# Performance work log

Hardware: AMD Instinct MI355X
Metric: run time of the kernel (lower is better)

Reference implementation:

```python
import jax, jax.numpy as jnp
import numpy as np

EXP_EMBD = 1024
EXP_Q_H = 8
EXP_HEAD_DIM = 256
EXP_KV_H = 1
EXP_KV_DIM = EXP_KV_H * EXP_HEAD_DIM  # 256
EXP_FFN = 4096
B, L, LC = 8, 512, 2048


def setup_inputs() -> dict:
    key = jax.random.key(0)
    ks = jax.random.split(key, 12)
    def w(k, shape):
        fan_in = shape[-1]
        return jax.random.normal(k, shape, jnp.float32) * (fan_in ** -0.5)
    return {
        "x": jax.random.normal(ks[0], (B, L, EXP_EMBD), jnp.float32),
        "text_k": jax.random.normal(ks[1], (B, LC, EXP_KV_DIM), jnp.float32),
        "text_v": jax.random.normal(ks[2], (B, LC, EXP_KV_DIM), jnp.float32),
        "ln1_w": jnp.ones((EXP_EMBD,), jnp.float32),
        "ln2_w": jnp.ones((EXP_EMBD,), jnp.float32),
        "Wq": w(ks[3], (EXP_Q_H * EXP_HEAD_DIM, EXP_EMBD)),
        "Wk": w(ks[4], (EXP_KV_DIM, EXP_KV_DIM)),
        "Wv": w(ks[5], (EXP_KV_DIM, EXP_KV_DIM)),
        "Wo": w(ks[6], (EXP_EMBD, EXP_Q_H * EXP_HEAD_DIM)),
        "Wg": w(ks[7], (EXP_FFN, EXP_EMBD)),
        "Wu": w(ks[8], (EXP_FFN, EXP_EMBD)),
        "Wd": w(ks[9], (EXP_EMBD, EXP_FFN)),
    }


def _rmsnorm(x, w):
    # torch.nn.RMSNorm with eps=None -> eps = finfo(dtype).eps
    eps = jnp.asarray(jnp.finfo(jnp.float32).eps, x.dtype)
    return x * jax.lax.rsqrt(jnp.mean(x * x, axis=-1, keepdims=True) + eps) * w


def _rope(x):
    # x: [B, L, H, D]
    b, l, h, d = x.shape
    d2 = d // 2
    ts = 10000.0 ** (2.0 / d * jnp.arange(d2, dtype=jnp.float32))  # [d2]
    rad = jnp.arange(l, dtype=jnp.float32)[:, None] / ts[None, :]  # [L, d2]
    s = jnp.sin(rad)[None, :, None, :]
    c = jnp.cos(rad)[None, :, None, :]
    x1, x2 = x[..., :d2], x[..., d2:]
    return jnp.concatenate([x1 * c - x2 * s, x2 * c + x1 * s], axis=-1)


def reference(x, text_k, text_v, ln1_w, ln2_w, Wq, Wk, Wv, Wo, Wg, Wu, Wd):
    b, l, _ = x.shape
    lc = text_k.shape[1]
    residual = x
    h = _rmsnorm(x, ln1_w)
    q = _rope((h @ Wq.T).reshape(b, l, EXP_Q_H, EXP_HEAD_DIM))          # [B,L,QH,D]
    k = (text_k @ Wk.T).reshape(b, lc, EXP_KV_H, EXP_HEAD_DIM)          # [B,Lc,KVH,D]
    v = (text_v @ Wv.T).reshape(b, lc, EXP_KV_H, EXP_HEAD_DIM)
    kv_map = (jnp.arange(EXP_Q_H) * EXP_KV_H) // EXP_Q_H                # GQA head map
    kh = jnp.take(k, kv_map, axis=2)                                    # [B,Lc,QH,D]
    vh = jnp.take(v, kv_map, axis=2)
    scale = 1.0 / np.sqrt(EXP_HEAD_DIM).astype(np.float32)
    scores = jnp.einsum('blhd,bchd->bhlc', q, kh) * scale               # [B,QH,L,Lc]
    attn = jax.nn.softmax(scores, axis=-1)
    ctx = jnp.einsum('bhlc,bchd->blhd', attn, vh).reshape(b, l, -1)
    x = ctx @ Wo.T + residual
    residual = x
    h = _rmsnorm(x, ln2_w)
    return (jax.nn.silu(h @ Wg.T) * (h @ Wu.T)) @ Wd.T + residual
```

## Files before the change

### kernel.cpp

```cpp
#include <hip/hip_runtime.h>

typedef __attribute__((ext_vector_type(4))) float f32x4;
typedef __attribute__((ext_vector_type(8))) short s16x8;
typedef __attribute__((ext_vector_type(4))) unsigned short u16x4;

#define B_    8
#define L_    512
#define LC_   2048
#define EMBD  1024

__device__ __forceinline__ float b2f(unsigned short u) {
  unsigned int i = ((unsigned int)u) << 16;
  float f; __builtin_memcpy(&f, &i, 4); return f;
}
__device__ __forceinline__ unsigned short f2b(float f) {
  unsigned int i; __builtin_memcpy(&i, &f, 4);
  unsigned int r = i + 0x7FFFu + ((i >> 16) & 1u);
  return (unsigned short)(r >> 16);
}

#define GLL16(g, l)                                                         \
  __builtin_amdgcn_global_load_lds(                                         \
      (__attribute__((address_space(1))) void*)(g),                         \
      (__attribute__((address_space(3))) void*)(l), 16, 0, 0)

#define VMCNT6() asm volatile("s_waitcnt vmcnt(6)" ::: "memory")
#define VMCNT0() asm volatile("s_waitcnt vmcnt(0)" ::: "memory")
#define LGKM0()  asm volatile("s_waitcnt lgkmcnt(0)" ::: "memory")

__global__ __launch_bounds__(256) void convert9(
    const float* s0, const float* s1, const float* s2, const float* s3,
    const float* s4, const float* s5, const float* s6, const float* s7,
    const float* s8,
    unsigned short* d0, unsigned short* d1, unsigned short* d2,
    unsigned short* d3, unsigned short* d4, unsigned short* d5,
    unsigned short* d6, unsigned short* d7, unsigned short* d8) {
  int bk = blockIdx.x;
  const float* s; unsigned short* d; int base;
  if      (bk <  2048) { s = s0; d = d0; base = 0; }
  else if (bk <  2112) { s = s1; d = d1; base = 2048; }
  else if (bk <  2176) { s = s2; d = d2; base = 2112; }
  else if (bk <  4224) { s = s3; d = d3; base = 2176; }
  else if (bk <  8320) { s = s4; d = d4; base = 4224; }
  else if (bk < 12416) { s = s5; d = d5; base = 8320; }
  else if (bk < 16512) { s = s6; d = d6; base = 12416; }
  else if (bk < 20608) { s = s7; d = d7; base = 16512; }
  else                 { s = s8; d = d8; base = 20608; }
  int i = (bk - base) * 256 + threadIdx.x;
  float4 v = ((const float4*)s)[i];
  u16x4 o = { f2b(v.x), f2b(v.y), f2b(v.z), f2b(v.w) };
  ((u16x4*)d)[i] = o;
}

__global__ __launch_bounds__(256) void rmsnorm_kernel(
    const float* __restrict__ x, const float* __restrict__ w,
    unsigned short* __restrict__ out) {
  int row = blockIdx.x;
  int tid = threadIdx.x;
  float4 v = ((const float4*)(x + (size_t)row * EMBD))[tid];
  float ss = v.x*v.x + v.y*v.y + v.z*v.z + v.w*v.w;
#pragma unroll
  for (int o = 1; o < 64; o <<= 1) ss += __shfl_xor(ss, o);
  __shared__ float red[4];
  if ((tid & 63) == 0) red[tid >> 6] = ss;
  __syncthreads();
  float tot = red[0] + red[1] + red[2] + red[3];
  float rs = rsqrtf(tot * (1.0f / EMBD) + 1.1920928955078125e-07f);
  float4 wv = ((const float4*)w)[tid];
  u16x4 o = { f2b(v.x*rs*wv.x), f2b(v.y*rs*wv.y), f2b(v.z*rs*wv.z), f2b(v.w*rs*wv.w) };
  ((u16x4*)(out + (size_t)row * EMBD))[tid] = o;
}

__global__ __launch_bounds__(256) void rope_kernel(unsigned short* __restrict__ q) {
  int idx = blockIdx.x * 256 + threadIdx.x;
  int i   = idx & 127;
  int h   = (idx >> 7) & 7;
  int row = idx >> 10;
  int l   = row & (L_ - 1);
  size_t base = (size_t)row * 2048 + h * 256 + i;
  float x1 = b2f(q[base]);
  float x2 = b2f(q[base + 128]);
  float ts  = powf(10000.0f, (float)i * (2.0f / 256.0f));
  float rad = (float)l / ts;
  float s, c;
  sincosf(rad, &s, &c);
  q[base]       = f2b(x1 * c - x2 * s);
  q[base + 128] = f2b(x2 * c + x1 * s);
}

__global__ __launch_bounds__(256) void act_kernel(
    const unsigned short* __restrict__ g, const unsigned short* __restrict__ u,
    unsigned short* __restrict__ out, int n8) {
  int i = blockIdx.x * 256 + threadIdx.x;
  if (i >= n8) return;
  s16x8 gv = ((const s16x8*)g)[i];
  s16x8 uv = ((const s16x8*)u)[i];
  s16x8 ov;
#pragma unroll
  for (int j = 0; j < 8; ++j) {
    float gf = b2f((unsigned short)gv[j]);
    float uf = b2f((unsigned short)uv[j]);
    float s  = gf / (1.0f + __expf(-gf));
    ov[j] = (short)f2b(s * uf);
  }
  ((s16x8*)out)[i] = ov;
}

template <int ADD_RES, int OUT_BF16>
__global__ __launch_bounds__(256, 2) void gemm_nt(
    const unsigned short* __restrict__ A, const unsigned short* __restrict__ Bw,
    const float* __restrict__ Res, void* __restrict__ C, int M, int N, int K) {
  __shared__ unsigned short As[128 * 64];
  __shared__ unsigned short Bs[128 * 64];
  const int tid = threadIdx.x;
  const int lane = tid & 63, wid = tid >> 6;
  const int l15 = lane & 15, l4 = lane >> 4;
  const int wr = wid >> 1, wc = wid & 1;
  const int m0 = blockIdx.y * 128, n0 = blockIdx.x * 128;

  const f32x4 fz = {0.f, 0.f, 0.f, 0.f};
  f32x4 acc[4][4];
#pragma unroll
  for (int i = 0; i < 4; ++i)
#pragma unroll
    for (int j = 0; j < 4; ++j) acc[i][j] = fz;

  for (int k0 = 0; k0 < K; k0 += 64) {
    __syncthreads();
#pragma unroll
    for (int i = 0; i < 4; ++i) {
      int Li = i * 4096 + tid * 16;
      int row = Li >> 7;
      int kb = (Li & 127) ^ ((row & 7) << 4);
      GLL16((const char*)(A + (size_t)(m0 + row) * K + k0) + kb, (char*)As + Li);
      GLL16((const char*)(Bw + (size_t)(n0 + row) * K + k0) + kb, (char*)Bs + Li);
    }
    __syncthreads();
#pragma unroll
    for (int kk = 0; kk < 2; ++kk) {
      s16x8 af[4], bfr[4];
#pragma unroll
      for (int mi = 0; mi < 4; ++mi) {
        int row = wr * 64 + mi * 16 + l15;
        int kb = (kk * 64 + l4 * 16) ^ ((row & 7) << 4);
        af[mi] = *(const s16x8*)((const char*)As + row * 128 + kb);
      }
#pragma unroll
      for (int ni = 0; ni < 4; ++ni) {
        int row = wc * 64 + ni * 16 + l15;
        int kb = (kk * 64 + l4 * 16) ^ ((row & 7) << 4);
        bfr[ni] = *(const s16x8*)((const char*)Bs + row * 128 + kb);
      }
#pragma unroll
      for (int mi = 0; mi < 4; ++mi)
#pragma unroll
        for (int ni = 0; ni < 4; ++ni)
          acc[mi][ni] = __builtin_amdgcn_mfma_f32_16x16x32_bf16(
              af[mi], bfr[ni], acc[mi][ni], 0, 0, 0);
    }
  }
#pragma unroll
  for (int mi = 0; mi < 4; ++mi) {
#pragma unroll
    for (int r = 0; r < 4; ++r) {
      int grow = m0 + wr * 64 + mi * 16 + l4 * 4 + r;
      size_t base = (size_t)grow * N + n0 + wc * 64 + l15;
#pragma unroll
      for (int ni = 0; ni < 4; ++ni) {
        float v = acc[mi][ni][r];
        size_t idx = base + ni * 16;
        if (ADD_RES) v += Res[idx];
        if (OUT_BF16) ((unsigned short*)C)[idx] = f2b(v);
        else          ((float*)C)[idx] = v;
      }
    }
  }
}

template <int ADD_RES, int OUT_BF16>
__global__ __launch_bounds__(256, 2) void gemm_nt64(
    const unsigned short* __restrict__ A, const unsigned short* __restrict__ Bw,
    const float* __restrict__ Res, void* __restrict__ C, int M, int N, int K) {
  __shared__ unsigned short As[64 * 64];
  __shared__ unsigned short Bs[128 * 64];
  const int tid = threadIdx.x;
  const int lane = tid & 63, wid = tid >> 6;
  const int l15 = lane & 15, l4 = lane >> 4;
  const int wr = wid >> 1, wc = wid & 1;
  const int m0 = blockIdx.y * 64, n0 = blockIdx.x * 128;

  const f32x4 fz = {0.f, 0.f, 0.f, 0.f};
  f32x4 acc[2][4];
#pragma unroll
  for (int i = 0; i < 2; ++i)
#pragma unroll
    for (int j = 0; j < 4; ++j) acc[i][j] = fz;

  for (int k0 = 0; k0 < K; k0 += 64) {
    __syncthreads();
#pragma unroll
    for (int i = 0; i < 2; ++i) {
      int Li = i * 4096 + tid * 16;
      int row = Li >> 7;
      int kb = (Li & 127) ^ ((row & 7) << 4);
      GLL16((const char*)(A + (size_t)(m0 + row) * K + k0) + kb, (char*)As + Li);
    }
#pragma unroll
    for (int i = 0; i < 4; ++i) {
      int Li = i * 4096 + tid * 16;
      int row = Li >> 7;
      int kb = (Li & 127) ^ ((row & 7) << 4);
      GLL16((const char*)(Bw + (size_t)(n0 + row) * K + k0) + kb, (char*)Bs + Li);
    }
    __syncthreads();
#pragma unroll
    for (int kk = 0; kk < 2; ++kk) {
      s16x8 af[2], bfr[4];
#pragma unroll
      for (int mi = 0; mi < 2; ++mi) {
        int row = wr * 32 + mi * 16 + l15;
        int kb = (kk * 64 + l4 * 16) ^ ((row & 7) << 4);
        af[mi] = *(const s16x8*)((const char*)As + row * 128 + kb);
      }
#pragma unroll
      for (int ni = 0; ni < 4; ++ni) {
        int row = wc * 64 + ni * 16 + l15;
        int kb = (kk * 64 + l4 * 16) ^ ((row & 7) << 4);
        bfr[ni] = *(const s16x8*)((const char*)Bs + row * 128 + kb);
      }
#pragma unroll
      for (int mi = 0; mi < 2; ++mi)
#pragma unroll
        for (int ni = 0; ni < 4; ++ni)
          acc[mi][ni] = __builtin_amdgcn_mfma_f32_16x16x32_bf16(
              af[mi], bfr[ni], acc[mi][ni], 0, 0, 0);
    }
  }
#pragma unroll
  for (int mi = 0; mi < 2; ++mi) {
#pragma unroll
    for (int r = 0; r < 4; ++r) {
      int grow = m0 + wr * 32 + mi * 16 + l4 * 4 + r;
      size_t base = (size_t)grow * N + n0 + wc * 64 + l15;
#pragma unroll
      for (int ni = 0; ni < 4; ++ni) {
        float v = acc[mi][ni][r];
        size_t idx = base + ni * 16;
        if (ADD_RES) v += Res[idx];
        if (OUT_BF16) ((unsigned short*)C)[idx] = f2b(v);
        else          ((float*)C)[idx] = v;
      }
    }
  }
}

__global__ __launch_bounds__(512, 2) void gemm256(
    const unsigned short* __restrict__ A, const unsigned short* __restrict__ Bw,
    unsigned short* __restrict__ C, int M, int N, int K) {
  extern __shared__ char smem[];
  const int tid = threadIdx.x;
  const int lane = tid & 63;
  const int wid = tid >> 6;
  const int wr = wid >> 2, wc = wid & 3;
  const int l15 = lane & 15, g = lane >> 4;
  int flat = blockIdx.y * 16 + blockIdx.x;
  flat = (flat & 7) * 32 + (flat >> 3);
  const int m0 = (flat >> 4) * 256, n0 = (flat & 15) * 256;
  const int T = K >> 6;
  const int swz = (l15 & 7) << 4;

  auto stage = [&](int t, int mat, int half) {
    char* dst = smem + mat * 65536 + (t & 1) * 32768 + half * 16384;
    const unsigned short* src = (mat ? Bw + (size_t)(n0 + half * 128) * K
                                     : A + (size_t)(m0 + half * 128) * K) + t * 64;
#pragma unroll
    for (int i = 0; i < 2; ++i) {
      int Li = i * 8192 + tid * 16;
      int row = Li >> 7;
      int kb = (Li & 127) ^ ((row & 7) << 4);
      GLL16((const char*)(src + (size_t)row * K) + kb, dst + Li);
    }
  };

  const f32x4 fz = {0.f, 0.f, 0.f, 0.f};
  f32x4 acc[2][2][4][2];
#pragma unroll
  for (int ms = 0; ms < 2; ++ms)
#pragma unroll
    for (int ns = 0; ns < 2; ++ns)
#pragma unroll
      for (int mi = 0; mi < 4; ++mi)
#pragma unroll
        for (int ni = 0; ni < 2; ++ni) acc[ms][ns][mi][ni] = fz;

  stage(0, 1, 0); stage(0, 1, 1); stage(0, 0, 0); stage(0, 0, 1);
  stage(1, 1, 0); stage(1, 1, 1); stage(1, 0, 0);
  VMCNT6();
  __builtin_amdgcn_s_barrier();

  for (int t = 0; t < T; ++t) {
    char* Ab = smem + (t & 1) * 32768 + wr * 16384;
    char* Bb = smem + 65536 + (t & 1) * 32768 + (wc >> 1) * 16384;
    const int bn = (wc & 1) * 64;
    s16x8 a[4][2], b0[2][2], b1[2][2];

#pragma unroll
    for (int mi = 0; mi < 4; ++mi) {
      int row = mi * 16 + l15;
#pragma unroll
      for (int kk = 0; kk < 2; ++kk)
        a[mi][kk] = *(const s16x8*)(Ab + row * 128 + ((kk * 64 + g * 16) ^ swz));
    }
#pragma unroll
    for (int ni = 0; ni < 2; ++ni) {
      int r0 = (bn + ni * 16 + l15) * 128;
      int r1 = (bn + 32 + ni * 16 + l15) * 128;
#pragma unroll
      for (int kk = 0; kk < 2; ++kk) {
        int ko = (kk * 64 + g * 16) ^ swz;
        b0[ni][kk] = *(const s16x8*)(Bb + r0 + ko);
        b1[ni][kk] = *(const s16x8*)(Bb + r1 + ko);
      }
    }
    if (t + 1 < T) stage(t + 1, 0, 1);
    __builtin_amdgcn_s_barrier();
    LGKM0();
    __builtin_amdgcn_sched_barrier(0);
    __builtin_amdgcn_s_setprio(1);
#pragma unroll
    for (int mi = 0; mi < 4; ++mi)
#pragma unroll
      for (int ni = 0; ni < 2; ++ni)
#pragma unroll
        for (int kk = 0; kk < 2; ++kk)
          acc[0][0][mi][ni] = __builtin_amdgcn_mfma_f32_16x16x32_bf16(
              a[mi][kk], b0[ni][kk], acc[0][0][mi][ni], 0, 0, 0);
    __builtin_amdgcn_s_setprio(0);
    __builtin_amdgcn_s_barrier();

    if (t + 2 < T) stage(t + 2, 1, 0);
    __builtin_amdgcn_s_barrier();
    __builtin_amdgcn_s_setprio(1);
#pragma unroll
    for (int mi = 0; mi < 4; ++mi)
#pragma unroll
      for (int ni = 0; ni < 2; ++ni)
#pragma unroll
        for (int kk = 0; kk < 2; ++kk)
          acc[0][1][mi][ni] = __builtin_amdgcn_mfma_f32_16x16x32_bf16(
              a[mi][kk], b1[ni][kk], acc[0][1][mi][ni], 0, 0, 0);
    __builtin_amdgcn_s_setprio(0);
    __builtin_amdgcn_s_barrier();

#pragma unroll
    for (int mi = 0; mi < 4; ++mi) {
      int row = 64 + mi * 16 + l15;
#pragma unroll
      for (int kk = 0; kk < 2; ++kk)
        a[mi][kk] = *(const s16x8*)(Ab + row * 128 + ((kk * 64 + g * 16) ^ swz));
    }
    if (t + 2 < T) stage(t + 2, 1, 1);
    __builtin_amdgcn_s_barrier();
    LGKM0();
    __builtin_amdgcn_sched_barrier(0);
    __builtin_amdgcn_s_setprio(1);
#pragma unroll
    for (int mi = 0; mi < 4; ++mi)
#pragma unroll
      for (int ni = 0; ni < 2; ++ni)
#pragma unroll
        for (int kk = 0; kk < 2; ++kk)
          acc[1][0][mi][ni] = __builtin_amdgcn_mfma_f32_16x16x32_bf16(
              a[mi][kk], b0[ni][kk], acc[1][0][mi][ni], 0, 0, 0);
    __builtin_amdgcn_s_setprio(0);
    __builtin_amdgcn_s_barrier();

    if (t + 2 < T) { stage(t + 2, 0, 0); VMCNT6(); }
    else           { VMCNT0(); }
    __builtin_amdgcn_s_barrier();
    __builtin_amdgcn_s_setprio(1);
#pragma unroll
    for (int mi = 0; mi < 4; ++mi)
#pragma unroll
      for (int ni = 0; ni < 2; ++ni)
#pragma unroll
        for (int kk = 0; kk < 2; ++kk)
          acc[1][1][mi][ni] = __builtin_amdgcn_mfma_f32_16x16x32_bf16(
              a[mi][kk], b1[ni][kk], acc[1][1][mi][ni], 0, 0, 0);
    __builtin_amdgcn_s_setprio(0);
    __builtin_amdgcn_s_barrier();
  }

#pragma unroll
  for (int ms = 0; ms < 2; ++ms)
#pragma unroll
    for (int mi = 0; mi < 4; ++mi)
#pragma unroll
      for (int r = 0; r < 4; ++r) {
        int grow = m0 + wr * 128 + ms * 64 + mi * 16 + g * 4 + r;
        size_t base = (size_t)grow * N + n0 + wc * 64;
#pragma unroll
        for (int ns = 0; ns < 2; ++ns)
#pragma unroll
          for (int ni = 0; ni < 2; ++ni)
            C[base + ns * 32 + ni * 16 + l15] = f2b(acc[ms][ns][mi][ni][r]);
      }
}

#define SWZV(d) (((((d) & 7) ^ (((d) >> 3) & 7))) << 4)

__global__ __launch_bounds__(512, 2) void attn_kernel(
    const unsigned short* __restrict__ Q,
    const unsigned short* __restrict__ Kc,
    const unsigned short* __restrict__ Vc,
    unsigned short* __restrict__ Op0, unsigned short* __restrict__ Op1,
    float2* __restrict__ Ml0, float2* __restrict__ Ml1) {
  __shared__ unsigned short Ks[64 * 256];
  __shared__ unsigned short Vt[256 * 64];
  const int tid = threadIdx.x;
  const int lane = tid & 63, wid = tid >> 6;
  const int l15 = lane & 15, g = lane >> 4;
  const int qt = blockIdx.x, h = blockIdx.y;
  const int b = blockIdx.z >> 1, half = blockIdx.z & 1;

  const size_t qrow = (size_t)(b * L_ + qt * 128 + wid * 16 + l15);
  const unsigned short* qp = Q + qrow * 2048 + h * 256;
  s16x8 qf[8];
#pragma unroll
  for (int kc = 0; kc < 8; ++kc) qf[kc] = *(const s16x8*)(qp + kc * 32 + g * 8);

  const f32x4 fz = {0.f, 0.f, 0.f, 0.f};
  f32x4 oacc[16];
#pragma unroll
  for (int i = 0; i < 16; ++i) oacc[i] = fz;
  float m_run = -__builtin_inff(), l_run = 0.f;

  const unsigned short* Kb = Kc + (size_t)b * LC_ * 256;
  const unsigned short* Vb = Vc + (size_t)b * LC_ * 256;

  const int kt0 = half * 16;
  for (int kt = kt0; kt < kt0 + 16; ++kt) {
    __syncthreads();
#pragma unroll
    for (int i = 0; i < 4; ++i) {
      int Li = i * 8192 + tid * 16;
      int row = Li >> 9;
      int kb = (Li & 511) ^ ((row & 7) << 4);
      GLL16((const char*)(Kb + (size_t)(kt * 64 + row) * 256) + kb, (char*)Ks + Li);
    }
#pragma unroll
    for (int p = 0; p < 2; ++p) {
      int id = p * 512 + tid;
      int dgrp = id & 31;
      int kvp = id >> 5;
      int d0 = dgrp * 8, kv0 = kvp * 2;
      const unsigned short* v0p = Vb + (size_t)(kt * 64 + kv0) * 256 + d0;
      s16x8 r0 = *(const s16x8*)v0p;
      s16x8 r1 = *(const s16x8*)(v0p + 256);
#pragma unroll
      for (int j = 0; j < 8; ++j) {
        int d = d0 + j;
        unsigned int val = (unsigned int)(unsigned short)r0[j] |
                           ((unsigned int)(unsigned short)r1[j] << 16);
        *(unsigned int*)((char*)Vt + d * 128 + ((kv0 * 2) ^ SWZV(d))) = val;
      }
    }
    __syncthreads();

    f32x4 sacc[4];
#pragma unroll
    for (int mi = 0; mi < 4; ++mi) sacc[mi] = fz;
#pragma unroll
    for (int mi = 0; mi < 4; ++mi) {
      int row = mi * 16 + l15;
      int swz = (row & 7) << 4;
#pragma unroll
      for (int kc = 0; kc < 8; ++kc) {
        s16x8 kf = *(const s16x8*)((const char*)Ks + row * 512 + ((kc * 64 + g * 16) ^ swz));
        sacc[mi] = __builtin_amdgcn_mfma_f32_16x16x32_bf16(kf, qf[kc], sacc[mi], 0, 0, 0);
      }
    }
    float sv[4][4];
    float mt = -__builtin_inff();
#pragma unroll
    for (int mi = 0; mi < 4; ++mi)
#pragma unroll
      for (int r = 0; r < 4; ++r) {
        float t = sacc[mi][r] * 0.0625f;
        sv[mi][r] = t;
        mt = fmaxf(mt, t);
      }
    mt = fmaxf(mt, __shfl_xor(mt, 16));
    mt = fmaxf(mt, __shfl_xor(mt, 32));
    if (!__all(mt <= m_run + 8.0f)) {
      float mnew = fmaxf(m_run, mt);
      float alpha = __expf(m_run - mnew);
      float af4[4];
#pragma unroll
      for (int r = 0; r < 4; ++r) af4[r] = __shfl(alpha, g * 4 + r);
#pragma unroll
      for (int nd = 0; nd < 16; ++nd)
#pragma unroll
        for (int r = 0; r < 4; ++r) oacc[nd][r] *= af4[r];
      l_run *= alpha;
      m_run = mnew;
    }
    float rs = 0.f;
#pragma unroll
    for (int mi = 0; mi < 4; ++mi)
#pragma unroll
      for (int r = 0; r < 4; ++r) {
        float p = __expf(sv[mi][r] - m_run);
        sv[mi][r] = p;
        rs += p;
      }
    rs += __shfl_xor(rs, 16);
    rs += __shfl_xor(rs, 32);
    l_run += rs;
    unsigned int pk[4][2];
#pragma unroll
    for (int ni = 0; ni < 4; ++ni) {
      pk[ni][0] = (unsigned int)f2b(sv[ni][0]) | ((unsigned int)f2b(sv[ni][1]) << 16);
      pk[ni][1] = (unsigned int)f2b(sv[ni][2]) | ((unsigned int)f2b(sv[ni][3]) << 16);
    }
    int cbase = (g & 1) << 3;
#pragma unroll
    for (int tt = 0; tt < 2; ++tt) {
      unsigned int w[4];
#pragma unroll
      for (int jj = 0; jj < 4; ++jj) {
        int c = cbase + (jj << 1);
        int src = ((c >> 2) << 4) + l15;
        unsigned int ra = __shfl(pk[2 * tt][jj & 1], src);
        unsigned int rb = __shfl(pk[2 * tt + 1][jj & 1], src);
        w[jj] = (g < 2) ? ra : rb;
      }
      union { unsigned int u[4]; s16x8 v; } cvt;
      cvt.u[0] = w[0]; cvt.u[1] = w[1]; cvt.u[2] = w[2]; cvt.u[3] = w[3];
      s16x8 ap = cvt.v;
#pragma unroll
      for (int nd = 0; nd < 16; ++nd) {
        int d = nd * 16 + l15;
        s16x8 vf = *(const s16x8*)((const char*)Vt + d * 128 + ((tt * 64 + g * 16) ^ SWZV(d)));
        oacc[nd] = __builtin_amdgcn_mfma_f32_16x16x32_bf16(ap, vf, oacc[nd], 0, 0, 0);
      }
    }
  }
  unsigned short* Op = half ? Op1 : Op0;
  float2* Ml = half ? Ml1 : Ml0;
  float lf[4];
#pragma unroll
  for (int r = 0; r < 4; ++r) lf[r] = 1.0f / __shfl(l_run, g * 4 + r);
  const size_t orow0 = (size_t)(b * L_ + qt * 128 + wid * 16);
#pragma unroll
  for (int r = 0; r < 4; ++r) {
    size_t base = (orow0 + g * 4 + r) * 2048 + h * 256 + l15;
#pragma unroll
    for (int nd = 0; nd < 16; ++nd)
      Op[base + nd * 16] = f2b(oacc[nd][r] * lf[r]);
  }
  if (g == 0) Ml[(orow0 + l15) * 8 + h] = make_float2(m_run, l_run);
}

__global__ __launch_bounds__(256) void attn_merge(
    const unsigned short* __restrict__ p0, const unsigned short* __restrict__ p1,
    const float2* __restrict__ ml0, const float2* __restrict__ ml1,
    unsigned short* __restrict__ ctx) {
  int i = blockIdx.x * 256 + threadIdx.x;
  int rowh = i >> 5;
  int dch = i & 31;
  float2 a = ml0[rowh], c = ml1[rowh];
  float M = fmaxf(a.x, c.x);
  float w0 = a.y * __expf(a.x - M), w1 = c.y * __expf(c.x - M);
  float inv = 1.0f / (w0 + w1);
  w0 *= inv; w1 *= inv;
  int row = rowh >> 3, h = rowh & 7;
  size_t off = (size_t)row * 2048 + h * 256 + dch * 8;
  s16x8 v0 = *(const s16x8*)(p0 + off);
  s16x8 v1 = *(const s16x8*)(p1 + off);
  s16x8 o;
#pragma unroll
  for (int j = 0; j < 8; ++j)
    o[j] = (short)f2b(w0 * b2f((unsigned short)v0[j]) + w1 * b2f((unsigned short)v1[j]));
  *(s16x8*)(ctx + off) = o;
}

extern "C" void kernel_launch(void* const* d_in, const int* in_sizes, int n_in,
                              void* d_out, int out_size, void* d_ws, size_t ws_size,
                              hipStream_t stream) {
  const float* x   = (const float*)d_in[0];
  const float* tk  = (const float*)d_in[1];
  const float* tv  = (const float*)d_in[2];
  const float* ln1 = (const float*)d_in[3];
  const float* ln2 = (const float*)d_in[4];
  const float* Wq  = (const float*)d_in[5];
  const float* Wk  = (const float*)d_in[6];
  const float* Wv  = (const float*)d_in[7];
  const float* Wo  = (const float*)d_in[8];
  const float* Wg  = (const float*)d_in[9];
  const float* Wu  = (const float*)d_in[10];
  const float* Wd  = (const float*)d_in[11];
  float* out = (float*)d_out;
  char* ws = (char*)d_ws;

  (void)hipFuncSetAttribute((const void*)gemm256,
                            hipFuncAttributeMaxDynamicSharedMemorySize, 131072);

  unsigned short* tk_bf  = (unsigned short*)(ws + 0);
  unsigned short* tv_bf  = (unsigned short*)(ws + 8388608);
  unsigned short* k_bf   = (unsigned short*)(ws + 16777216);
  unsigned short* v_bf   = (unsigned short*)(ws + 25165824);
  unsigned short* g_bf   = (unsigned short*)(ws + 0);
  unsigned short* op0    = (unsigned short*)(ws + 0);
  unsigned short* q_bf   = (unsigned short*)(ws + 33554432);
  unsigned short* ctx_bf = (unsigned short*)(ws + 50331648);
  unsigned short* u_bf   = (unsigned short*)(ws + 33554432);
  unsigned short* wq_bf  = (unsigned short*)(ws + 67108864);
  unsigned short* wk_bf  = (unsigned short*)(ws + 71303168);
  unsigned short* wv_bf  = (unsigned short*)(ws + 71434240);
  unsigned short* wo_bf  = (unsigned short*)(ws + 71565312);
  unsigned short* wg_bf  = (unsigned short*)(ws + 75759616);
  unsigned short* wu_bf  = (unsigned short*)(ws + 84148224);
  unsigned short* wd_bf  = (unsigned short*)(ws + 92536832);
  unsigned short* h_bf   = (unsigned short*)(ws + 100925440);
  float2*         ml0    = (float2*)(ws + 100925440);
  float2*         ml1    = (float2*)(ws + 100925440 + 262144);
  float*          x2     = (float*)(ws + 109314048);
  unsigned short* op1    = (unsigned short*)(ws + 109314048);

  dim3 blk(256);
  convert9<<<dim3(24704), blk, 0, stream>>>(
      Wq, Wk, Wv, Wo, Wg, Wu, Wd, tk, tv,
      wq_bf, wk_bf, wv_bf, wo_bf, wg_bf, wu_bf, wd_bf, tk_bf, tv_bf);

  rmsnorm_kernel<<<dim3(4096), blk, 0, stream>>>(x, ln1, h_bf);
  gemm_nt<0, 1><<<dim3(16, 32), blk, 0, stream>>>(h_bf, wq_bf, nullptr, q_bf, 4096, 2048, 1024);
  rope_kernel<<<dim3(16384), blk, 0, stream>>>(q_bf);
  gemm_nt64<0, 1><<<dim3(2, 256), blk, 0, stream>>>(tk_bf, wk_bf, nullptr, k_bf, 16384, 256, 256);
  gemm_nt64<0, 1><<<dim3(2, 256), blk, 0, stream>>>(tv_bf, wv_bf, nullptr, v_bf, 16384, 256, 256);
  attn_kernel<<<dim3(4, 8, 16), dim3(512), 0, stream>>>(q_bf, k_bf, v_bf, op0, op1, ml0, ml1);
  attn_merge<<<dim3(4096), blk, 0, stream>>>(op0, op1, ml0, ml1, ctx_bf);
  gemm_nt64<1, 0><<<dim3(8, 64), blk, 0, stream>>>(ctx_bf, wo_bf, x, x2, 4096, 1024, 2048);
  rmsnorm_kernel<<<dim3(4096), blk, 0, stream>>>(x2, ln2, h_bf);
  gemm256<<<dim3(16, 16), dim3(512), 131072, stream>>>(h_bf, wg_bf, g_bf, 4096, 4096, 1024);
  gemm256<<<dim3(16, 16), dim3(512), 131072, stream>>>(h_bf, wu_bf, u_bf, 4096, 4096, 1024);
  act_kernel<<<dim3(8192), blk, 0, stream>>>(g_bf, u_bf, g_bf, 2097152);
  gemm_nt64<1, 0><<<dim3(8, 64), blk, 0, stream>>>(g_bf, wd_bf, x2, out, 4096, 1024, 4096);
}
```

Before: 411.6 us.

## Process two 16-row query tiles per wave in attention kernel with 256 threads

Each attention wave now handles 32 query rows, two independent 16-row tiles, instead of 16. The workgroup shrinks from 512 to 256 threads, so the same 128-row block is covered by half as many waves. Each K and V fragment read from LDS now feeds two MFMAs, halving LDS read traffic per unit of compute and giving independent MFMA chains to interleave. The cost is roughly double the accumulator registers per wave (two 16x256 output tiles), which may hurt occupancy or cause spills, and each thread now does twice as many global loads for K and V per tile.

```diff
diff --git a/kernel.cpp b/kernel.cpp
--- a/kernel.cpp
+++ b/kernel.cpp
@@ -409,7 +409,7 @@
 
 #define SWZV(d) (((((d) & 7) ^ (((d) >> 3) & 7))) << 4)
 
-__global__ __launch_bounds__(512, 2) void attn_kernel(
+__global__ __launch_bounds__(256, 2) void attn_kernel(
     const unsigned short* __restrict__ Q,
     const unsigned short* __restrict__ Kc,
     const unsigned short* __restrict__ Vc,
@@ -423,17 +423,22 @@
   const int qt = blockIdx.x, h = blockIdx.y;
   const int b = blockIdx.z >> 1, half = blockIdx.z & 1;
 
-  const size_t qrow = (size_t)(b * L_ + qt * 128 + wid * 16 + l15);
-  const unsigned short* qp = Q + qrow * 2048 + h * 256;
-  s16x8 qf[8];
-#pragma unroll
-  for (int kc = 0; kc < 8; ++kc) qf[kc] = *(const s16x8*)(qp + kc * 32 + g * 8);
+  const size_t qrowA = (size_t)(b * L_ + qt * 128 + wid * 32 + l15);
+  const unsigned short* qpA = Q + qrowA * 2048 + h * 256;
+  const unsigned short* qpB = qpA + 16 * 2048;
+  s16x8 qfA[8], qfB[8];
+#pragma unroll
+  for (int kc = 0; kc < 8; ++kc) {
+    qfA[kc] = *(const s16x8*)(qpA + kc * 32 + g * 8);
+    qfB[kc] = *(const s16x8*)(qpB + kc * 32 + g * 8);
+  }
 
   const f32x4 fz = {0.f, 0.f, 0.f, 0.f};
-  f32x4 oacc[16];
-#pragma unroll
-  for (int i = 0; i < 16; ++i) oacc[i] = fz;
-  float m_run = -__builtin_inff(), l_run = 0.f;
+  f32x4 oaccA[16], oaccB[16];
+#pragma unroll
+  for (int i = 0; i < 16; ++i) { oaccA[i] = fz; oaccB[i] = fz; }
+  float m_runA = -__builtin_inff(), l_runA = 0.f;
+  float m_runB = -__builtin_inff(), l_runB = 0.f;
 
   const unsigned short* Kb = Kc + (size_t)b * LC_ * 256;
   const unsigned short* Vb = Vc + (size_t)b * LC_ * 256;
@@ -442,15 +447,15 @@
   for (int kt = kt0; kt < kt0 + 16; ++kt) {
     __syncthreads();
 #pragma unroll
-    for (int i = 0; i < 4; ++i) {
-      int Li = i * 8192 + tid * 16;
+    for (int i = 0; i < 8; ++i) {
+      int Li = i * 4096 + tid * 16;
       int row = Li >> 9;
       int kb = (Li & 511) ^ ((row & 7) << 4);
       GLL16((const char*)(Kb + (size_t)(kt * 64 + row) * 256) + kb, (char*)Ks + Li);
     }
 #pragma unroll
-    for (int p = 0; p < 2; ++p) {
-      int id = p * 512 + tid;
+    for (int p = 0; p < 4; ++p) {
+      int id = p * 256 + tid;
       int dgrp = id & 31;
       int kvp = id >> 5;
       int d0 = dgrp * 8, kv0 = kvp * 2;
@@ -467,9 +472,9 @@
     }
     __syncthreads();
 
-    f32x4 sacc[4];
-#pragma unroll
-    for (int mi = 0; mi < 4; ++mi) sacc[mi] = fz;
+    f32x4 sA[4], sB[4];
+#pragma unroll
+    for (int mi = 0; mi < 4; ++mi) { sA[mi] = fz; sB[mi] = fz; }
 #pragma unroll
     for (int mi = 0; mi < 4; ++mi) {
       int row = mi * 16 + l15;
@@ -477,89 +482,152 @@
 #pragma unroll
       for (int kc = 0; kc < 8; ++kc) {
         s16x8 kf = *(const s16x8*)((const char*)Ks + row * 512 + ((kc * 64 + g * 16) ^ swz));
-        sacc[mi] = __builtin_amdgcn_mfma_f32_16x16x32_bf16(kf, qf[kc], sacc[mi], 0, 0, 0);
-      }
-    }
-    float sv[4][4];
-    float mt = -__builtin_inff();
-#pragma unroll
-    for (int mi = 0; mi < 4; ++mi)
-#pragma unroll
-      for (int r = 0; r < 4; ++r) {
-        float t = sacc[mi][r] * 0.0625f;
-        sv[mi][r] = t;
-        mt = fmaxf(mt, t);
-      }
-    mt = fmaxf(mt, __shfl_xor(mt, 16));
-    mt = fmaxf(mt, __shfl_xor(mt, 32));
-    if (!__all(mt <= m_run + 8.0f)) {
-      float mnew = fmaxf(m_run, mt);
-      float alpha = __expf(m_run - mnew);
-      float af4[4];
-#pragma unroll
-      for (int r = 0; r < 4; ++r) af4[r] = __shfl(alpha, g * 4 + r);
-#pragma unroll
-      for (int nd = 0; nd < 16; ++nd)
-#pragma unroll
-        for (int r = 0; r < 4; ++r) oacc[nd][r] *= af4[r];
-      l_run *= alpha;
-      m_run = mnew;
-    }
-    float rs = 0.f;
-#pragma unroll
-    for (int mi = 0; mi < 4; ++mi)
-#pragma unroll
-      for (int r = 0; r < 4; ++r) {
-        float p = __expf(sv[mi][r] - m_run);
-        sv[mi][r] = p;
-        rs += p;
-      }
-    rs += __shfl_xor(rs, 16);
-    rs += __shfl_xor(rs, 32);
-    l_run += rs;
-    unsigned int pk[4][2];
-#pragma unroll
-    for (int ni = 0; ni < 4; ++ni) {
-      pk[ni][0] = (unsigned int)f2b(sv[ni][0]) | ((unsigned int)f2b(sv[ni][1]) << 16);
-      pk[ni][1] = (unsigned int)f2b(sv[ni][2]) | ((unsigned int)f2b(sv[ni][3]) << 16);
-    }
+        sA[mi] = __builtin_amdgcn_mfma_f32_16x16x32_bf16(kf, qfA[kc], sA[mi], 0, 0, 0);
+        sB[mi] = __builtin_amdgcn_mfma_f32_16x16x32_bf16(kf, qfB[kc], sB[mi], 0, 0, 0);
+      }
+    }
+
+    float svA[4][4], svB[4][4];
+    unsigned int pkA[4][2], pkB[4][2];
+    {
+      float mt = -__builtin_inff();
+#pragma unroll
+      for (int mi = 0; mi < 4; ++mi)
+#pragma unroll
+        for (int r = 0; r < 4; ++r) {
+          float t = sA[mi][r] * 0.0625f;
+          svA[mi][r] = t;
+          mt = fmaxf(mt, t);
+        }
+      mt = fmaxf(mt, __shfl_xor(mt, 16));
+      mt = fmaxf(mt, __shfl_xor(mt, 32));
+      if (!__all(mt <= m_runA + 8.0f)) {
+        float mnew = fmaxf(m_runA, mt);
+        float alpha = __expf(m_runA - mnew);
+        float af4[4];
+#pragma unroll
+        for (int r = 0; r < 4; ++r) af4[r] = __shfl(alpha, g * 4 + r);
+#pragma unroll
+        for (int nd = 0; nd < 16; ++nd)
+#pragma unroll
+          for (int r = 0; r < 4; ++r) oaccA[nd][r] *= af4[r];
+        l_runA *= alpha;
+        m_runA = mnew;
+      }
+      float rs = 0.f;
+#pragma unroll
+      for (int mi = 0; mi < 4; ++mi)
+#pragma unroll
+        for (int r = 0; r < 4; ++r) {
+          float p = __expf(svA[mi][r] - m_runA);
+          svA[mi][r] = p;
+          rs += p;
+        }
+      rs += __shfl_xor(rs, 16);
+      rs += __shfl_xor(rs, 32);
+      l_runA += rs;
+#pragma unroll
+      for (int ni = 0; ni < 4; ++ni) {
+        pkA[ni][0] = (unsigned int)f2b(svA[ni][0]) | ((unsigned int)f2b(svA[ni][1]) << 16);
+        pkA[ni][1] = (unsigned int)f2b(svA[ni][2]) | ((unsigned int)f2b(svA[ni][3]) << 16);
+      }
+    }
+    {
+      float mt = -__builtin_inff();
+#pragma unroll
+      for (int mi = 0; mi < 4; ++mi)
+#pragma unroll
+        for (int r = 0; r < 4; ++r) {
+          float t = sB[mi][r] * 0.0625f;
+          svB[mi][r] = t;
+          mt = fmaxf(mt, t);
+        }
+      mt = fmaxf(mt, __shfl_xor(mt, 16));
+      mt = fmaxf(mt, __shfl_xor(mt, 32));
+      if (!__all(mt <= m_runB + 8.0f)) {
+        float mnew = fmaxf(m_runB, mt);
+        float alpha = __expf(m_runB - mnew);
+        float af4[4];
+#pragma unroll
+        for (int r = 0; r < 4; ++r) af4[r] = __shfl(alpha, g * 4 + r);
+#pragma unroll
+        for (int nd = 0; nd < 16; ++nd)
+#pragma unroll
+          for (int r = 0; r < 4; ++r) oaccB[nd][r] *= af4[r];
+        l_runB *= alpha;
+        m_runB = mnew;
+      }
+      float rs = 0.f;
+#pragma unroll
+      for (int mi = 0; mi < 4; ++mi)
+#pragma unroll
+        for (int r = 0; r < 4; ++r) {
+          float p = __expf(svB[mi][r] - m_runB);
+          svB[mi][r] = p;
+          rs += p;
+        }
+      rs += __shfl_xor(rs, 16);
+      rs += __shfl_xor(rs, 32);
+      l_runB += rs;
+#pragma unroll
+      for (int ni = 0; ni < 4; ++ni) {
+        pkB[ni][0] = (unsigned int)f2b(svB[ni][0]) | ((unsigned int)f2b(svB[ni][1]) << 16);
+        pkB[ni][1] = (unsigned int)f2b(svB[ni][2]) | ((unsigned int)f2b(svB[ni][3]) << 16);
+      }
+    }
+
     int cbase = (g & 1) << 3;
 #pragma unroll
     for (int tt = 0; tt < 2; ++tt) {
-      unsigned int w[4];
+      unsigned int wA[4], wB[4];
 #pragma unroll
       for (int jj = 0; jj < 4; ++jj) {
         int c = cbase + (jj << 1);
         int src = ((c >> 2) << 4) + l15;
-        unsigned int ra = __shfl(pk[2 * tt][jj & 1], src);
-        unsigned int rb = __shfl(pk[2 * tt + 1][jj & 1], src);
-        w[jj] = (g < 2) ? ra : rb;
-      }
-      union { unsigned int u[4]; s16x8 v; } cvt;
-      cvt.u[0] = w[0]; cvt.u[1] = w[1]; cvt.u[2] = w[2]; cvt.u[3] = w[3];
-      s16x8 ap = cvt.v;
+        unsigned int raA = __shfl(pkA[2 * tt][jj & 1], src);
+        unsigned int rbA = __shfl(pkA[2 * tt + 1][jj & 1], src);
+        wA[jj] = (g < 2) ? raA : rbA;
+        unsigned int raB = __shfl(pkB[2 * tt][jj & 1], src);
+        unsigned int rbB = __shfl(pkB[2 * tt + 1][jj & 1], src);
+        wB[jj] = (g < 2) ? raB : rbB;
+      }
+      union { unsigned int u[4]; s16x8 v; } cvA, cvB;
+      cvA.u[0] = wA[0]; cvA.u[1] = wA[1]; cvA.u[2] = wA[2]; cvA.u[3] = wA[3];
+      cvB.u[0] = wB[0]; cvB.u[1] = wB[1]; cvB.u[2] = wB[2]; cvB.u[3] = wB[3];
+      s16x8 apA = cvA.v, apB = cvB.v;
 #pragma unroll
       for (int nd = 0; nd < 16; ++nd) {
         int d = nd * 16 + l15;
         s16x8 vf = *(const s16x8*)((const char*)Vt + d * 128 + ((tt * 64 + g * 16) ^ SWZV(d)));
-        oacc[nd] = __builtin_amdgcn_mfma_f32_16x16x32_bf16(ap, vf, oacc[nd], 0, 0, 0);
+        oaccA[nd] = __builtin_amdgcn_mfma_f32_16x16x32_bf16(apA, vf, oaccA[nd], 0, 0, 0);
+        oaccB[nd] = __builtin_amdgcn_mfma_f32_16x16x32_bf16(apB, vf, oaccB[nd], 0, 0, 0);
       }
     }
   }
   unsigned short* Op = half ? Op1 : Op0;
   float2* Ml = half ? Ml1 : Ml0;
-  float lf[4];
-#pragma unroll
-  for (int r = 0; r < 4; ++r) lf[r] = 1.0f / __shfl(l_run, g * 4 + r);
-  const size_t orow0 = (size_t)(b * L_ + qt * 128 + wid * 16);
+  const size_t orow0A = (size_t)(b * L_ + qt * 128 + wid * 32);
+  const size_t orow0B = orow0A + 16;
+  float lfA[4], lfB[4];
 #pragma unroll
   for (int r = 0; r < 4; ++r) {
-    size_t base = (orow0 + g * 4 + r) * 2048 + h * 256 + l15;
-#pragma unroll
-    for (int nd = 0; nd < 16; ++nd)
-      Op[base + nd * 16] = f2b(oacc[nd][r] * lf[r]);
-  }
-  if (g == 0) Ml[(orow0 + l15) * 8 + h] = make_float2(m_run, l_run);
+    lfA[r] = 1.0f / __shfl(l_runA, g * 4 + r);
+    lfB[r] = 1.0f / __shfl(l_runB, g * 4 + r);
+  }
+#pragma unroll
+  for (int r = 0; r < 4; ++r) {
+    size_t baseA = (orow0A + g * 4 + r) * 2048 + h * 256 + l15;
+    size_t baseB = (orow0B + g * 4 + r) * 2048 + h * 256 + l15;
+#pragma unroll
+    for (int nd = 0; nd < 16; ++nd) {
+      Op[baseA + nd * 16] = f2b(oaccA[nd][r] * lfA[r]);
+      Op[baseB + nd * 16] = f2b(oaccB[nd][r] * lfB[r]);
+    }
+  }
+  if (g == 0) {
+    Ml[(orow0A + l15) * 8 + h] = make_float2(m_runA, l_runA);
+    Ml[(orow0B + l15) * 8 + h] = make_float2(m_runB, l_runB);
+  }
 }
 
 __global__ __launch_bounds__(256) void attn_merge(
@@ -638,7 +706,7 @@
   rope_kernel<<<dim3(16384), blk, 0, stream>>>(q_bf);
   gemm_nt64<0, 1><<<dim3(2, 256), blk, 0, stream>>>(tk_bf, wk_bf, nullptr, k_bf, 16384, 256, 256);
   gemm_nt64<0, 1><<<dim3(2, 256), blk, 0, stream>>>(tv_bf, wv_bf, nullptr, v_bf, 16384, 256, 256);
-  attn_kernel<<<dim3(4, 8, 16), dim3(512), 0, stream>>>(q_bf, k_bf, v_bf, op0, op1, ml0, ml1);
+  attn_kernel<<<dim3(4, 8, 16), dim3(256), 0, stream>>>(q_bf, k_bf, v_bf, op0, op1, ml0, ml1);
   attn_merge<<<dim3(4096), blk, 0, stream>>>(op0, op1, ml0, ml1, ctx_bf);
   gemm_nt64<1, 0><<<dim3(8, 64), blk, 0, stream>>>(ctx_bf, wo_bf, x, x2, 4096, 1024, 2048);
   rmsnorm_kernel<<<dim3(4096), blk, 0, stream>>>(x2, ln2, h_bf);
```

Measured after the change: 688.1 us. +67.2%, slower.

## Double-buffer K/V tiles in attention and fuse SwiGLU into up-projection GEMM epilogue

Applied to the files above, without the earlier changes.

The attention kernel now uses 128KB of dynamic shared memory with two K and two V tile buffers. The next tile's K is fetched asynchronously and its V is loaded into registers while the current tile's MFMAs run, leaving one barrier per iteration. Separately, the SiLU-gate multiply moves into the epilogue of the up-projection GEMM, which reads the gate output and overwrites it in place. This drops the standalone activation kernel and one bf16 intermediate round trip. The larger shared memory footprint may cut attention occupancy from two blocks per CU to one.

```diff
diff --git a/kernel.cpp b/kernel.cpp
--- a/kernel.cpp
+++ b/kernel.cpp
@@ -88,24 +88,6 @@
   q[base + 128] = f2b(x2 * c + x1 * s);
 }
 
-__global__ __launch_bounds__(256) void act_kernel(
-    const unsigned short* __restrict__ g, const unsigned short* __restrict__ u,
-    unsigned short* __restrict__ out, int n8) {
-  int i = blockIdx.x * 256 + threadIdx.x;
-  if (i >= n8) return;
-  s16x8 gv = ((const s16x8*)g)[i];
-  s16x8 uv = ((const s16x8*)u)[i];
-  s16x8 ov;
-#pragma unroll
-  for (int j = 0; j < 8; ++j) {
-    float gf = b2f((unsigned short)gv[j]);
-    float uf = b2f((unsigned short)uv[j]);
-    float s  = gf / (1.0f + __expf(-gf));
-    ov[j] = (short)f2b(s * uf);
-  }
-  ((s16x8*)out)[i] = ov;
-}
-
 template <int ADD_RES, int OUT_BF16>
 __global__ __launch_bounds__(256, 2) void gemm_nt(
     const unsigned short* __restrict__ A, const unsigned short* __restrict__ Bw,
@@ -254,9 +236,11 @@
   }
 }
 
+template <int SWIGLU>
 __global__ __launch_bounds__(512, 2) void gemm256(
     const unsigned short* __restrict__ A, const unsigned short* __restrict__ Bw,
-    unsigned short* __restrict__ C, int M, int N, int K) {
+    const unsigned short* __restrict__ G, unsigned short* __restrict__ C,
+    int M, int N, int K) {
   extern __shared__ char smem[];
   const int tid = threadIdx.x;
   const int lane = tid & 63;
@@ -402,8 +386,15 @@
 #pragma unroll
         for (int ns = 0; ns < 2; ++ns)
 #pragma unroll
-          for (int ni = 0; ni < 2; ++ni)
-            C[base + ns * 32 + ni * 16 + l15] = f2b(acc[ms][ns][mi][ni][r]);
+          for (int ni = 0; ni < 2; ++ni) {
+            size_t idx = base + ns * 32 + ni * 16 + l15;
+            float v = acc[ms][ns][mi][ni][r];
+            if (SWIGLU) {
+              float gf = b2f(G[idx]);
+              v *= gf / (1.0f + __expf(-gf));
+            }
+            C[idx] = f2b(v);
+          }
       }
 }
 
@@ -415,8 +406,7 @@
     const unsigned short* __restrict__ Vc,
     unsigned short* __restrict__ Op0, unsigned short* __restrict__ Op1,
     float2* __restrict__ Ml0, float2* __restrict__ Ml1) {
-  __shared__ unsigned short Ks[64 * 256];
-  __shared__ unsigned short Vt[256 * 64];
+  extern __shared__ char ats[];
   const int tid = threadIdx.x;
   const int lane = tid & 63, wid = tid >> 6;
   const int l15 = lane & 15, g = lane >> 4;
@@ -438,34 +428,55 @@
   const unsigned short* Kb = Kc + (size_t)b * LC_ * 256;
   const unsigned short* Vb = Vc + (size_t)b * LC_ * 256;
 
-  const int kt0 = half * 16;
-  for (int kt = kt0; kt < kt0 + 16; ++kt) {
-    __syncthreads();
+  auto stageK = [&](int kt, char* dstK) {
 #pragma unroll
     for (int i = 0; i < 4; ++i) {
       int Li = i * 8192 + tid * 16;
       int row = Li >> 9;
       int kb = (Li & 511) ^ ((row & 7) << 4);
-      GLL16((const char*)(Kb + (size_t)(kt * 64 + row) * 256) + kb, (char*)Ks + Li);
-    }
+      GLL16((const char*)(Kb + (size_t)(kt * 64 + row) * 256) + kb, dstK + Li);
+    }
+  };
+  s16x8 vr[2][2];
+  auto loadV = [&](int kt) {
 #pragma unroll
     for (int p = 0; p < 2; ++p) {
       int id = p * 512 + tid;
-      int dgrp = id & 31;
-      int kvp = id >> 5;
+      int dgrp = id & 31, kvp = id >> 5;
+      const unsigned short* v0p = Vb + (size_t)(kt * 64 + kvp * 2) * 256 + dgrp * 8;
+      vr[p][0] = *(const s16x8*)v0p;
+      vr[p][1] = *(const s16x8*)(v0p + 256);
+    }
+  };
+  auto writeV = [&](char* dstV) {
+#pragma unroll
+    for (int p = 0; p < 2; ++p) {
+      int id = p * 512 + tid;
+      int dgrp = id & 31, kvp = id >> 5;
       int d0 = dgrp * 8, kv0 = kvp * 2;
-      const unsigned short* v0p = Vb + (size_t)(kt * 64 + kv0) * 256 + d0;
-      s16x8 r0 = *(const s16x8*)v0p;
-      s16x8 r1 = *(const s16x8*)(v0p + 256);
 #pragma unroll
       for (int j = 0; j < 8; ++j) {
         int d = d0 + j;
-        unsigned int val = (unsigned int)(unsigned short)r0[j] |
-                           ((unsigned int)(unsigned short)r1[j] << 16);
-        *(unsigned int*)((char*)Vt + d * 128 + ((kv0 * 2) ^ SWZV(d))) = val;
-      }
-    }
-    __syncthreads();
+        unsigned int val = (unsigned int)(unsigned short)vr[p][0][j] |
+                           ((unsigned int)(unsigned short)vr[p][1][j] << 16);
+        *(unsigned int*)(dstV + d * 128 + ((kv0 * 2) ^ SWZV(d))) = val;
+      }
+    }
+  };
+
+  const int kt0 = half * 16, ktE = kt0 + 16;
+  stageK(kt0, ats);
+  loadV(kt0);
+  VMCNT0();
+  writeV(ats + 65536);
+  __syncthreads();
+
+  for (int kt = kt0; kt < ktE; ++kt) {
+    const int cur = (kt - kt0) & 1, nxt = cur ^ 1;
+    char* KsB = ats + cur * 32768;
+    char* VtB = ats + 65536 + cur * 32768;
+    const bool more = (kt + 1 < ktE);
+    if (more) { stageK(kt + 1, ats + nxt * 32768); loadV(kt + 1); }
 
     f32x4 sacc[4];
 #pragma unroll
@@ -476,7 +487,7 @@
       int swz = (row & 7) << 4;
 #pragma unroll
       for (int kc = 0; kc < 8; ++kc) {
-        s16x8 kf = *(const s16x8*)((const char*)Ks + row * 512 + ((kc * 64 + g * 16) ^ swz));
+        s16x8 kf = *(const s16x8*)(KsB + row * 512 + ((kc * 64 + g * 16) ^ swz));
         sacc[mi] = __builtin_amdgcn_mfma_f32_16x16x32_bf16(kf, qf[kc], sacc[mi], 0, 0, 0);
       }
     }
@@ -541,10 +552,13 @@
 #pragma unroll
       for (int nd = 0; nd < 16; ++nd) {
         int d = nd * 16 + l15;
-        s16x8 vf = *(const s16x8*)((const char*)Vt + d * 128 + ((tt * 64 + g * 16) ^ SWZV(d)));
+        s16x8 vf = *(const s16x8*)(VtB + d * 128 + ((tt * 64 + g * 16) ^ SWZV(d)));
         oacc[nd] = __builtin_amdgcn_mfma_f32_16x16x32_bf16(ap, vf, oacc[nd], 0, 0, 0);
       }
     }
+
+    if (more) { VMCNT0(); writeV(ats + 65536 + nxt * 32768); }
+    __syncthreads();
   }
   unsigned short* Op = half ? Op1 : Op0;
   float2* Ml = half ? Ml1 : Ml0;
@@ -603,7 +617,11 @@
   float* out = (float*)d_out;
   char* ws = (char*)d_ws;
 
-  (void)hipFuncSetAttribute((const void*)gemm256,
+  (void)hipFuncSetAttribute((const void*)gemm256<0>,
+                            hipFuncAttributeMaxDynamicSharedMemorySize, 131072);
+  (void)hipFuncSetAttribute((const void*)gemm256<1>,
+                            hipFuncAttributeMaxDynamicSharedMemorySize, 131072);
+  (void)hipFuncSetAttribute((const void*)attn_kernel,
                             hipFuncAttributeMaxDynamicSharedMemorySize, 131072);
 
   unsigned short* tk_bf  = (unsigned short*)(ws + 0);
@@ -638,12 +656,11 @@
   rope_kernel<<<dim3(16384), blk, 0, stream>>>(q_bf);
   gemm_nt64<0, 1><<<dim3(2, 256), blk, 0, stream>>>(tk_bf, wk_bf, nullptr, k_bf, 16384, 256, 256);
   gemm_nt64<0, 1><<<dim3(2, 256), blk, 0, stream>>>(tv_bf, wv_bf, nullptr, v_bf, 16384, 256, 256);
-  attn_kernel<<<dim3(4, 8, 16), dim3(512), 0, stream>>>(q_bf, k_bf, v_bf, op0, op1, ml0, ml1);
+  attn_kernel<<<dim3(4, 8, 16), dim3(512), 131072, stream>>>(q_bf, k_bf, v_bf, op0, op1, ml0, ml1);
   attn_merge<<<dim3(4096), blk, 0, stream>>>(op0, op1, ml0, ml1, ctx_bf);
   gemm_nt64<1, 0><<<dim3(8, 64), blk, 0, stream>>>(ctx_bf, wo_bf, x, x2, 4096, 1024, 2048);
   rmsnorm_kernel<<<dim3(4096), blk, 0, stream>>>(x2, ln2, h_bf);
-  gemm256<<<dim3(16, 16), dim3(512), 131072, stream>>>(h_bf, wg_bf, g_bf, 4096, 4096, 1024);
-  gemm256<<<dim3(16, 16), dim3(512), 131072, stream>>>(h_bf, wu_bf, u_bf, 4096, 4096, 1024);
-  act_kernel<<<dim3(8192), blk, 0, stream>>>(g_bf, u_bf, g_bf, 2097152);
+  gemm256<0><<<dim3(16, 16), dim3(512), 131072, stream>>>(h_bf, wg_bf, nullptr, g_bf, 4096, 4096, 1024);
+  gemm256<1><<<dim3(16, 16), dim3(512), 131072, stream>>>(h_bf, wu_bf, g_bf, g_bf, 4096, 4096, 1024);
   gemm_nt64<1, 0><<<dim3(8, 64), blk, 0, stream>>>(g_bf, wd_bf, x2, out, 4096, 1024, 4096);
 }
```

Measured after the change: 400.4 us. -2.7%, faster.

## Fuse SwiGLU into up-projection GEMM epilogue and transpose attention PV MFMA

Applied to the files above, without the earlier changes.

The separate SiLU-multiply kernel is removed. The up-projection GEMM epilogue now reads the gate output, applies SiLU and writes the product in place, which saves a full read/write pass over the 4096x4096 intermediate and one launch. In attention, K rows are loaded in a permuted order so that the score accumulator layout matches the PV MFMA operand directly. The PV MFMA now computes O transposed, which removes the cross-lane shuffles for P, alpha and l, and lets the output use 4-element vector stores. The in-place gate/up aliasing and the K permutation both depend on the layouts matching exactly.

```diff
diff --git a/kernel.cpp b/kernel.cpp
--- a/kernel.cpp
+++ b/kernel.cpp
@@ -88,24 +88,6 @@
   q[base + 128] = f2b(x2 * c + x1 * s);
 }
 
-__global__ __launch_bounds__(256) void act_kernel(
-    const unsigned short* __restrict__ g, const unsigned short* __restrict__ u,
-    unsigned short* __restrict__ out, int n8) {
-  int i = blockIdx.x * 256 + threadIdx.x;
-  if (i >= n8) return;
-  s16x8 gv = ((const s16x8*)g)[i];
-  s16x8 uv = ((const s16x8*)u)[i];
-  s16x8 ov;
-#pragma unroll
-  for (int j = 0; j < 8; ++j) {
-    float gf = b2f((unsigned short)gv[j]);
-    float uf = b2f((unsigned short)uv[j]);
-    float s  = gf / (1.0f + __expf(-gf));
-    ov[j] = (short)f2b(s * uf);
-  }
-  ((s16x8*)out)[i] = ov;
-}
-
 template <int ADD_RES, int OUT_BF16>
 __global__ __launch_bounds__(256, 2) void gemm_nt(
     const unsigned short* __restrict__ A, const unsigned short* __restrict__ Bw,
@@ -254,9 +236,11 @@
   }
 }
 
+template <int SWIGLU>
 __global__ __launch_bounds__(512, 2) void gemm256(
     const unsigned short* __restrict__ A, const unsigned short* __restrict__ Bw,
-    unsigned short* __restrict__ C, int M, int N, int K) {
+    const unsigned short* __restrict__ G, unsigned short* __restrict__ C,
+    int M, int N, int K) {
   extern __shared__ char smem[];
   const int tid = threadIdx.x;
   const int lane = tid & 63;
@@ -402,8 +386,15 @@
 #pragma unroll
         for (int ns = 0; ns < 2; ++ns)
 #pragma unroll
-          for (int ni = 0; ni < 2; ++ni)
-            C[base + ns * 32 + ni * 16 + l15] = f2b(acc[ms][ns][mi][ni][r]);
+          for (int ni = 0; ni < 2; ++ni) {
+            size_t idx = base + ns * 32 + ni * 16 + l15;
+            float v = acc[ms][ns][mi][ni][r];
+            if (SWIGLU) {
+              float gf = b2f(G[idx]);
+              v *= gf / (1.0f + __expf(-gf));
+            }
+            C[idx] = f2b(v);
+          }
       }
 }
 
@@ -438,22 +429,23 @@
   const unsigned short* Kb = Kc + (size_t)b * LC_ * 256;
   const unsigned short* Vb = Vc + (size_t)b * LC_ * 256;
 
-  const int kt0 = half * 16;
-  for (int kt = kt0; kt < kt0 + 16; ++kt) {
+  const int kt0 = half * 16, ktE = kt0 + 16;
+  for (int kt = kt0; kt < ktE; ++kt) {
     __syncthreads();
 #pragma unroll
     for (int i = 0; i < 4; ++i) {
       int Li = i * 8192 + tid * 16;
       int row = Li >> 9;
+      int mi = row >> 4;
+      int kvp = ((mi >> 1) << 5) | (((row >> 2) & 3) << 3) | ((mi & 1) << 2) | (row & 3);
       int kb = (Li & 511) ^ ((row & 7) << 4);
-      GLL16((const char*)(Kb + (size_t)(kt * 64 + row) * 256) + kb, (char*)Ks + Li);
+      GLL16((const char*)(Kb + (size_t)(kt * 64 + kvp) * 256) + kb, (char*)Ks + Li);
     }
 #pragma unroll
     for (int p = 0; p < 2; ++p) {
       int id = p * 512 + tid;
-      int dgrp = id & 31;
-      int kvp = id >> 5;
-      int d0 = dgrp * 8, kv0 = kvp * 2;
+      int dgrp = id & 31, kvp2 = id >> 5;
+      int d0 = dgrp * 8, kv0 = kvp2 * 2;
       const unsigned short* v0p = Vb + (size_t)(kt * 64 + kv0) * 256 + d0;
       s16x8 r0 = *(const s16x8*)v0p;
       s16x8 r1 = *(const s16x8*)(v0p + 256);
@@ -495,13 +487,10 @@
     if (!__all(mt <= m_run + 8.0f)) {
       float mnew = fmaxf(m_run, mt);
       float alpha = __expf(m_run - mnew);
-      float af4[4];
-#pragma unroll
-      for (int r = 0; r < 4; ++r) af4[r] = __shfl(alpha, g * 4 + r);
 #pragma unroll
       for (int nd = 0; nd < 16; ++nd)
 #pragma unroll
-        for (int r = 0; r < 4; ++r) oacc[nd][r] *= af4[r];
+        for (int r = 0; r < 4; ++r) oacc[nd][r] *= alpha;
       l_run *= alpha;
       m_run = mnew;
     }
@@ -523,41 +512,31 @@
       pk[ni][0] = (unsigned int)f2b(sv[ni][0]) | ((unsigned int)f2b(sv[ni][1]) << 16);
       pk[ni][1] = (unsigned int)f2b(sv[ni][2]) | ((unsigned int)f2b(sv[ni][3]) << 16);
     }
-    int cbase = (g & 1) << 3;
 #pragma unroll
     for (int tt = 0; tt < 2; ++tt) {
-      unsigned int w[4];
-#pragma unroll
-      for (int jj = 0; jj < 4; ++jj) {
-        int c = cbase + (jj << 1);
-        int src = ((c >> 2) << 4) + l15;
-        unsigned int ra = __shfl(pk[2 * tt][jj & 1], src);
-        unsigned int rb = __shfl(pk[2 * tt + 1][jj & 1], src);
-        w[jj] = (g < 2) ? ra : rb;
-      }
-      union { unsigned int u[4]; s16x8 v; } cvt;
-      cvt.u[0] = w[0]; cvt.u[1] = w[1]; cvt.u[2] = w[2]; cvt.u[3] = w[3];
-      s16x8 ap = cvt.v;
+      union { unsigned int u[4]; s16x8 v; } pf;
+      pf.u[0] = pk[2 * tt][0];
+      pf.u[1] = pk[2 * tt][1];
+      pf.u[2] = pk[2 * tt + 1][0];
+      pf.u[3] = pk[2 * tt + 1][1];
 #pragma unroll
       for (int nd = 0; nd < 16; ++nd) {
         int d = nd * 16 + l15;
         s16x8 vf = *(const s16x8*)((const char*)Vt + d * 128 + ((tt * 64 + g * 16) ^ SWZV(d)));
-        oacc[nd] = __builtin_amdgcn_mfma_f32_16x16x32_bf16(ap, vf, oacc[nd], 0, 0, 0);
+        oacc[nd] = __builtin_amdgcn_mfma_f32_16x16x32_bf16(vf, pf.v, oacc[nd], 0, 0, 0);
       }
     }
   }
   unsigned short* Op = half ? Op1 : Op0;
   float2* Ml = half ? Ml1 : Ml0;
-  float lf[4];
-#pragma unroll
-  for (int r = 0; r < 4; ++r) lf[r] = 1.0f / __shfl(l_run, g * 4 + r);
+  float lf = 1.0f / l_run;
   const size_t orow0 = (size_t)(b * L_ + qt * 128 + wid * 16);
-#pragma unroll
-  for (int r = 0; r < 4; ++r) {
-    size_t base = (orow0 + g * 4 + r) * 2048 + h * 256 + l15;
-#pragma unroll
-    for (int nd = 0; nd < 16; ++nd)
-      Op[base + nd * 16] = f2b(oacc[nd][r] * lf[r]);
+  const size_t base = (orow0 + l15) * 2048 + h * 256 + g * 4;
+#pragma unroll
+  for (int nd = 0; nd < 16; ++nd) {
+    u16x4 o = { f2b(oacc[nd][0] * lf), f2b(oacc[nd][1] * lf),
+                f2b(oacc[nd][2] * lf), f2b(oacc[nd][3] * lf) };
+    *(u16x4*)(Op + base + nd * 16) = o;
   }
   if (g == 0) Ml[(orow0 + l15) * 8 + h] = make_float2(m_run, l_run);
 }
@@ -603,7 +582,9 @@
   float* out = (float*)d_out;
   char* ws = (char*)d_ws;
 
-  (void)hipFuncSetAttribute((const void*)gemm256,
+  (void)hipFuncSetAttribute((const void*)gemm256<0>,
+                            hipFuncAttributeMaxDynamicSharedMemorySize, 131072);
+  (void)hipFuncSetAttribute((const void*)gemm256<1>,
                             hipFuncAttributeMaxDynamicSharedMemorySize, 131072);
 
   unsigned short* tk_bf  = (unsigned short*)(ws + 0);
@@ -642,8 +623,7 @@
   attn_merge<<<dim3(4096), blk, 0, stream>>>(op0, op1, ml0, ml1, ctx_bf);
   gemm_nt64<1, 0><<<dim3(8, 64), blk, 0, stream>>>(ctx_bf, wo_bf, x, x2, 4096, 1024, 2048);
   rmsnorm_kernel<<<dim3(4096), blk, 0, stream>>>(x2, ln2, h_bf);
-  gemm256<<<dim3(16, 16), dim3(512), 131072, stream>>>(h_bf, wg_bf, g_bf, 4096, 4096, 1024);
-  gemm256<<<dim3(16, 16), dim3(512), 131072, stream>>>(h_bf, wu_bf, u_bf, 4096, 4096, 1024);
-  act_kernel<<<dim3(8192), blk, 0, stream>>>(g_bf, u_bf, g_bf, 2097152);
+  gemm256<0><<<dim3(16, 16), dim3(512), 131072, stream>>>(h_bf, wg_bf, nullptr, g_bf, 4096, 4096, 1024);
+  gemm256<1><<<dim3(16, 16), dim3(512), 131072, stream>>>(h_bf, wu_bf, g_bf, g_bf, 4096, 4096, 1024);
   gemm_nt64<1, 0><<<dim3(8, 64), blk, 0, stream>>>(g_bf, wd_bf, x2, out, 4096, 1024, 4096);
 }
```

Measured after the change: 392.1 us. -4.7%, faster.
